# Optimization experiments

Measured on AMD Instinct MI355X. Metric: run time of the kernel, lower is better.

The kernel has to match this reference:

```python
import jax, jax.numpy as jnp
import numpy as np

N_NODES = 8192
D = 384
N_EDGES = 262144
N_REL = 4
N_LAYERS = 2
BATCH = 64


def setup_inputs() -> dict:
    key = jax.random.key(0)
    ks = jax.random.split(key, 8)
    x = jax.random.normal(ks[0], (N_NODES, D), jnp.float32)
    edge_index = jax.random.randint(ks[1], (2, N_EDGES), 0, N_NODES, dtype=jnp.int32)
    edge_type = jax.random.randint(ks[2], (N_EDGES,), 0, N_REL, dtype=jnp.int32)
    s = 1.0 / np.sqrt(D)
    W_rel = jax.random.uniform(ks[3], (N_LAYERS, N_REL, D, D), jnp.float32, -s, s)
    b_rel = jnp.zeros((N_LAYERS, N_REL, D), jnp.float32)
    norm_const = jnp.ones((N_LAYERS, N_REL), jnp.float32)
    W_msg = jax.random.uniform(ks[4], (N_LAYERS, D, D), jnp.float32, -s, s)
    b_msg = jnp.zeros((N_LAYERS, D), jnp.float32)
    W_self = jax.random.uniform(ks[5], (N_LAYERS, D, D), jnp.float32, -s, s)
    b_self = jnp.zeros((N_LAYERS, D), jnp.float32)
    bn_gamma = jnp.ones((D,), jnp.float32)
    bn_beta = jnp.zeros((D,), jnp.float32)
    return {"x": x, "edge_index": edge_index, "edge_type": edge_type,
            "bn_gamma": bn_gamma, "bn_beta": bn_beta,
            "W_rel": W_rel, "b_rel": b_rel, "norm_const": norm_const,
            "W_msg": W_msg, "b_msg": b_msg, "W_self": W_self, "b_self": b_self,
            "batch_size": BATCH}


def _seg_sum(v, idx, n):
    return jax.ops.segment_sum(v, idx, num_segments=n)


def _forward(x, bn_gamma, bn_beta, W_rel, b_rel, norm_const, W_msg, b_msg,
             W_self, b_self, edge_index, edge_type, batch_size):
    n = x.shape[0]
    # BatchNorm1d (training-mode batch stats) on the utterance embeddings
    mu = x.mean(axis=0)
    var = x.var(axis=0)
    h = bn_gamma * (x - mu) * jax.lax.rsqrt(var + 1e-5) + bn_beta
    src, dst = edge_index[0], edge_index[1]  # PyG: row=source(j), col=target(i)
    # pairwise cosine similarity, gathered only at the edges actually used:
    # edge_weights[dst, src] = <h_dst, h_src> / (|h_dst||h_src|)
    xn = h / jnp.linalg.norm(h, axis=1, keepdims=True)
    w_e = jnp.sum(xn[dst] * xn[src], axis=-1)  # [E]
    ones_e = jnp.ones(src.shape[0], jnp.float32)
    n_layers, n_rel = W_rel.shape[0], W_rel.shape[1]
    for l in range(n_layers):
        # RelationAwareMP: per-relation linear + weighted scatter-mean, summed
        out = jnp.zeros((n, W_rel.shape[2]), h.dtype)
        for r in range(n_rel):
            mask = (edge_type == r).astype(h.dtype)  # [E]
            xr = h @ W_rel[l, r].T + b_rel[l, r]  # [N, D]
            coef = mask * w_e / norm_const[l, r]  # [E]
            s = _seg_sum(coef[:, None] * xr[src], dst, n)
            c = _seg_sum(mask, dst, n)
            out = out + s / jnp.maximum(c, 1.0)[:, None]
        rel_out = jax.nn.relu(out)
        # MP: relu(mean_j lin(x_j) + self_lin(x)), then residual
        mj = rel_out @ W_msg[l].T + b_msg[l]
        s = _seg_sum(mj[src], dst, n)
        c = _seg_sum(ones_e, dst, n)
        aggr = s / jnp.maximum(c, 1.0)[:, None]
        h = jax.nn.relu(aggr + rel_out @ W_self[l].T + b_self[l]) + h
    return h.reshape(batch_size, -1, h.shape[-1]).mean(axis=1)


def reference(x, edge_index, edge_type, bn_gamma, bn_beta, W_rel, b_rel,
              norm_const, W_msg, b_msg, W_self, b_self, batch_size):
    return _forward(x, bn_gamma, bn_beta, W_rel, b_rel, norm_const,
                    W_msg, b_msg, W_self, b_self,
                    edge_index, edge_type, batch_size)
```

## Files before the change

### kernel.cpp

```cpp
#include <hip/hip_runtime.h>
#include <hip/hip_bf16.h>

#define NN 8192
#define DD 384
#define NE 262144
#define NR 4
#define NL 2
#define NB 64

typedef __attribute__((ext_vector_type(8))) short bf16x8;
typedef __attribute__((ext_vector_type(4))) float f32x4;

__device__ __forceinline__ unsigned short f2bf(float f) {
  unsigned u = __float_as_uint(f);
  unsigned r = (u + 0x7fffu + ((u >> 16) & 1u)) >> 16;
  return (unsigned short)r;
}
__device__ __forceinline__ unsigned pack_bf2(float lo, float hi) {
  return (unsigned)f2bf(lo) | ((unsigned)f2bf(hi) << 16);
}
__device__ __forceinline__ float bflo(unsigned u) { return __uint_as_float(u << 16); }
__device__ __forceinline__ float bfhi(unsigned u) { return __uint_as_float(u & 0xffff0000u); }
__device__ __forceinline__ void gl_lds16(const void* g, void* l) {
  __builtin_amdgcn_global_load_lds(
      (const __attribute__((address_space(1))) unsigned int*)g,
      (__attribute__((address_space(3))) unsigned int*)l, 16, 0, 0);
}
__device__ __forceinline__ float dot8(uint4 a, uint4 b) {
  return bflo(a.x) * bflo(b.x) + bfhi(a.x) * bfhi(b.x) +
         bflo(a.y) * bflo(b.y) + bfhi(a.y) * bfhi(b.y) +
         bflo(a.z) * bflo(b.z) + bfhi(a.z) * bfhi(b.z) +
         bflo(a.w) * bflo(b.w) + bfhi(a.w) * bfhi(b.w);
}

__global__ void k_colstats(const float* __restrict__ x, float* __restrict__ musum,
                           float* __restrict__ msqsum) {
  int c = threadIdx.x;
  int r0 = blockIdx.x * 32;
  float s = 0.f, s2 = 0.f;
  for (int r = 0; r < 32; ++r) {
    float v = x[(size_t)(r0 + r) * DD + c];
    s += v; s2 += v * v;
  }
  atomicAdd(&musum[c], s);
  atomicAdd(&msqsum[c], s2);
}

__global__ void k_bn(const float* __restrict__ x, const float* __restrict__ gamma,
                     const float* __restrict__ beta, const float* __restrict__ musum,
                     const float* __restrict__ msqsum, float* __restrict__ h,
                     short* __restrict__ h_bf, float* __restrict__ ninv) {
  int n = blockIdx.x;
  int t = threadIdx.x;
  float ss = 0.f;
#pragma unroll
  for (int i = 0; i < 6; ++i) {
    int c = t + i * 64;
    float m = musum[c] * (1.f / NN);
    float var = msqsum[c] * (1.f / NN) - m * m;
    float v = gamma[c] * (x[(size_t)n * DD + c] - m) * rsqrtf(var + 1e-5f) + beta[c];
    h[(size_t)n * DD + c] = v;
    h_bf[(size_t)n * DD + c] = (short)f2bf(v);
    ss += v * v;
  }
#pragma unroll
  for (int m = 32; m; m >>= 1) ss += __shfl_xor(ss, m, 64);
  if (t == 0) ninv[n] = rsqrtf(ss);
}

__global__ void k_counts(const int* __restrict__ ei, const int* __restrict__ et,
                         int* __restrict__ c_rel) {
  int e = blockIdx.x * blockDim.x + threadIdx.x;
  if (e >= NE) return;
  int dst = ei[NE + e];
  atomicAdd(&c_rel[dst * NR + et[e]], 1);
}

__global__ void k_scan(const int* __restrict__ c_rel, int* __restrict__ rp2,
                       int* __restrict__ cursor) {
  __shared__ int part[1024];
  int t = threadIdx.x;
  int base = t * 32;
  int v[32]; int s = 0;
#pragma unroll
  for (int i = 0; i < 32; ++i) { v[i] = c_rel[base + i]; s += v[i]; }
  part[t] = s;
  __syncthreads();
  for (int off = 1; off < 1024; off <<= 1) {
    int add = (t >= off) ? part[t - off] : 0;
    __syncthreads();
    part[t] += add;
    __syncthreads();
  }
  int run = (t == 0) ? 0 : part[t - 1];
  if (t == 0) rp2[0] = 0;
#pragma unroll
  for (int i = 0; i < 32; ++i) {
    cursor[base + i] = run;
    run += v[i];
    rp2[base + i + 1] = run;
  }
}

__global__ void k_we(const short* __restrict__ hb, const float* __restrict__ ninv,
                     const int* __restrict__ ei, float* __restrict__ w_e) {
  int sl = threadIdx.x & 15;
  int grp = (blockIdx.x * blockDim.x + threadIdx.x) >> 4;
  int ngrp = (gridDim.x * blockDim.x) >> 4;
  for (int e = grp; e < NE; e += ngrp) {
    int s = ei[e], d = ei[NE + e];
    const uint4* hs = (const uint4*)(hb + (size_t)s * DD);
    const uint4* hd = (const uint4*)(hb + (size_t)d * DD);
    uint4 a0 = hs[sl], a1 = hs[16 + sl], a2 = hs[32 + sl];
    uint4 b0 = hd[sl], b1 = hd[16 + sl], b2 = hd[32 + sl];
    float acc = dot8(a0, b0) + dot8(a1, b1) + dot8(a2, b2);
#pragma unroll
    for (int m = 8; m; m >>= 1) acc += __shfl_xor(acc, m, 64);
    if (sl == 0) w_e[e] = acc * ninv[s] * ninv[d];
  }
}

__global__ void k_fill(const int* __restrict__ ei, const int* __restrict__ et,
                       const float* __restrict__ w_e, int* __restrict__ cursor,
                       int* __restrict__ meta, float* __restrict__ wsort) {
  int e = blockIdx.x * blockDim.x + threadIdx.x;
  if (e >= NE) return;
  int src = ei[e], dst = ei[NE + e];
  int pos = atomicAdd(&cursor[dst * NR + et[e]], 1);
  meta[pos] = src;
  wsort[pos] = w_e[e];
}

__global__ void k_aggrel(const short* __restrict__ hb, const int* __restrict__ rp2,
                         const int* __restrict__ meta, const float* __restrict__ wsort,
                         const float* __restrict__ nc, short* __restrict__ Agg,
                         float* __restrict__ SC, int layer) {
  int n = blockIdx.x;
  int t = threadIdx.x;
  int r = t / 96;
  int i = t - r * 96;
  int beg = rp2[n * 4 + r], end = rp2[n * 4 + r + 1];
  float a0 = 0, a1 = 0, a2 = 0, a3 = 0, s = 0;
  int e = beg;
  for (; e + 3 < end; e += 4) {
    int s0 = meta[e], s1 = meta[e + 1], s2 = meta[e + 2], s3 = meta[e + 3];
    float w0 = wsort[e], w1 = wsort[e + 1], w2 = wsort[e + 2], w3 = wsort[e + 3];
    uint2 u0 = ((const uint2*)(hb + (size_t)s0 * DD))[i];
    uint2 u1 = ((const uint2*)(hb + (size_t)s1 * DD))[i];
    uint2 u2 = ((const uint2*)(hb + (size_t)s2 * DD))[i];
    uint2 u3 = ((const uint2*)(hb + (size_t)s3 * DD))[i];
    a0 += w0 * bflo(u0.x) + w1 * bflo(u1.x) + w2 * bflo(u2.x) + w3 * bflo(u3.x);
    a1 += w0 * bfhi(u0.x) + w1 * bfhi(u1.x) + w2 * bfhi(u2.x) + w3 * bfhi(u3.x);
    a2 += w0 * bflo(u0.y) + w1 * bflo(u1.y) + w2 * bflo(u2.y) + w3 * bflo(u3.y);
    a3 += w0 * bfhi(u0.y) + w1 * bfhi(u1.y) + w2 * bfhi(u2.y) + w3 * bfhi(u3.y);
    s += w0 + w1 + w2 + w3;
  }
  for (; e < end; ++e) {
    int s0 = meta[e];
    float w0 = wsort[e];
    uint2 u0 = ((const uint2*)(hb + (size_t)s0 * DD))[i];
    a0 += w0 * bflo(u0.x); a1 += w0 * bfhi(u0.x);
    a2 += w0 * bflo(u0.y); a3 += w0 * bfhi(u0.y);
    s += w0;
  }
  int c = end - beg;
  float f = 1.f / (nc[layer * 4 + r] * (float)(c > 1 ? c : 1));
  uint2 o;
  o.x = pack_bf2(a0 * f, a1 * f);
  o.y = pack_bf2(a2 * f, a3 * f);
  ((uint2*)(Agg + (size_t)n * 1536 + r * 384))[i] = o;
  if (i == 0) SC[n * 4 + r] = s * f;
}

__global__ void k_aggmp(short* __restrict__ B1, const int* __restrict__ rp2,
                        const int* __restrict__ meta) {
  __shared__ float red[3][96][4];
  int n = blockIdx.x;
  int t = threadIdx.x;
  int g = t / 96, i = t - g * 96;
  int beg = rp2[n * 4], end = rp2[n * 4 + 4];
  float a0 = 0, a1 = 0, a2 = 0, a3 = 0;
  int e = beg + g;
  for (; e + 12 < end; e += 16) {
    int s0 = meta[e], s1 = meta[e + 4], s2 = meta[e + 8], s3 = meta[e + 12];
    uint2 u0 = ((const uint2*)(B1 + (size_t)s0 * 768 + 384))[i];
    uint2 u1 = ((const uint2*)(B1 + (size_t)s1 * 768 + 384))[i];
    uint2 u2 = ((const uint2*)(B1 + (size_t)s2 * 768 + 384))[i];
    uint2 u3 = ((const uint2*)(B1 + (size_t)s3 * 768 + 384))[i];
    a0 += bflo(u0.x) + bflo(u1.x) + bflo(u2.x) + bflo(u3.x);
    a1 += bfhi(u0.x) + bfhi(u1.x) + bfhi(u2.x) + bfhi(u3.x);
    a2 += bflo(u0.y) + bflo(u1.y) + bflo(u2.y) + bflo(u3.y);
    a3 += bfhi(u0.y) + bfhi(u1.y) + bfhi(u2.y) + bfhi(u3.y);
  }
  for (; e < end; e += 4) {
    int s0 = meta[e];
    uint2 u = ((const uint2*)(B1 + (size_t)s0 * 768 + 384))[i];
    a0 += bflo(u.x); a1 += bfhi(u.x);
    a2 += bflo(u.y); a3 += bfhi(u.y);
  }
  if (g) {
    red[g - 1][i][0] = a0; red[g - 1][i][1] = a1;
    red[g - 1][i][2] = a2; red[g - 1][i][3] = a3;
  }
  __syncthreads();
  if (g == 0) {
#pragma unroll
    for (int k = 0; k < 3; ++k) {
      a0 += red[k][i][0]; a1 += red[k][i][1];
      a2 += red[k][i][2]; a3 += red[k][i][3];
    }
    float inv = (end > beg) ? 1.f / (float)(end - beg) : 0.f;
    uint2 o;
    o.x = pack_bf2(a0 * inv, a1 * inv);
    o.y = pack_bf2(a2 * inv, a3 * inv);
    ((uint2*)(B1 + (size_t)n * 768))[i] = o;
  }
}

__global__ void k_packall(const float* __restrict__ W_rel, const float* __restrict__ W_msg,
                          const float* __restrict__ W_self, short* __restrict__ Wcat,
                          short* __restrict__ Wcat2) {
  const int T1 = NL * 384 * 1536;
  const int T2 = NL * 384 * 768;
  int idx = blockIdx.x * blockDim.x + threadIdx.x;
  if (idx < T1) {
    int l = idx / (384 * 1536);
    int rem = idx - l * 384 * 1536;
    int i = rem / 1536, kk = rem - i * 1536;
    int r = kk / 384, k = kk - r * 384;
    Wcat[idx] = (short)f2bf(W_rel[(((size_t)(l * NR + r) * DD) + i) * DD + k]);
  } else if (idx < T1 + T2) {
    int j = idx - T1;
    int l = j / (384 * 768);
    int rem = j - l * 384 * 768;
    int i = rem / 768, kk = rem - i * 768;
    float v = (kk < 384) ? W_msg[((size_t)l * DD + i) * DD + kk]
                         : W_self[((size_t)l * DD + i) * DD + kk - 384];
    Wcat2[j] = (short)f2bf(v);
  }
}

template <int MODE>
__global__ __launch_bounds__(256) void k_gemm_mfma(
    const short* __restrict__ A, int K, const short* __restrict__ Bp,
    const float* __restrict__ SC, const float* __restrict__ brel_l,
    const float* __restrict__ bmsg_l, const float* __restrict__ bself_l,
    const int* __restrict__ rp2, float* __restrict__ h,
    short* __restrict__ h_bf, short* __restrict__ Cout) {
  __shared__ short As[64 * 32];
  __shared__ short Bs[64 * 32];
  int tid = threadIdx.x;
  int lane = tid & 63;
  int w = tid >> 6;
  int wr = w >> 1, wc = w & 1;
  int bm = blockIdx.x, bn = blockIdx.y;

  const short* Ag = A + (size_t)(bm * 64 + (tid >> 2)) * K + (tid & 3) * 8;
  const short* Bg = Bp + (size_t)(bn * 64 + (tid >> 2)) * K + (tid & 3) * 8;
  short* Asl = As + w * 512;
  short* Bsl = Bs + w * 512;

  f32x4 acc[2][2] = {};
  int fr = lane & 15, fk = (lane >> 4) * 8;
  for (int k0 = 0; k0 < K; k0 += 32) {
    __syncthreads();
    gl_lds16(Ag + k0, Asl);
    gl_lds16(Bg + k0, Bsl);
    __syncthreads();
    bf16x8 a[2], b[2];
#pragma unroll
    for (int i = 0; i < 2; ++i)
      a[i] = *(const bf16x8*)&As[(wr * 32 + i * 16 + fr) * 32 + fk];
#pragma unroll
    for (int j = 0; j < 2; ++j)
      b[j] = *(const bf16x8*)&Bs[(wc * 32 + j * 16 + fr) * 32 + fk];
#pragma unroll
    for (int i = 0; i < 2; ++i)
#pragma unroll
      for (int j = 0; j < 2; ++j)
        acc[i][j] = __builtin_amdgcn_mfma_f32_16x16x32_bf16(a[i], b[j], acc[i][j], 0, 0, 0);
  }

  int cr = (lane >> 4) * 4;
  int cc = lane & 15;
#pragma unroll
  for (int i = 0; i < 2; ++i) {
#pragma unroll
    for (int jj = 0; jj < 4; ++jj) {
      int row = bm * 64 + wr * 32 + i * 16 + cr + jj;
      if (MODE == 0) {
        float4 sc = *(const float4*)&SC[row * 4];
#pragma unroll
        for (int j = 0; j < 2; ++j) {
          int col = bn * 64 + wc * 32 + j * 16 + cc;
          float v = acc[i][j][jj] + sc.x * brel_l[col] + sc.y * brel_l[384 + col] +
                    sc.z * brel_l[768 + col] + sc.w * brel_l[1152 + col];
          Cout[(size_t)row * 768 + 384 + col] = (short)f2bf(fmaxf(v, 0.f));
        }
      } else {
        float bmul = (rp2[(row + 1) * 4] > rp2[row * 4]) ? 1.f : 0.f;
#pragma unroll
        for (int j = 0; j < 2; ++j) {
          int col = bn * 64 + wc * 32 + j * 16 + cc;
          float v = acc[i][j][jj] + bmul * bmsg_l[col] + bself_l[col];
          float o = fmaxf(v, 0.f) + h[(size_t)row * DD + col];
          h[(size_t)row * DD + col] = o;
          h_bf[(size_t)row * DD + col] = (short)f2bf(o);
        }
      }
    }
  }
}

__global__ void k_out(const float* __restrict__ h, float* __restrict__ out) {
  int b = blockIdx.x;
  int c = threadIdx.x;
  float s = 0.f;
  for (int j = 0; j < 128; ++j) s += h[(size_t)(b * 128 + j) * DD + c];
  out[b * DD + c] = s * (1.f / 128.f);
}

extern "C" void kernel_launch(void* const* d_in, const int* in_sizes, int n_in,
                              void* d_out, int out_size, void* d_ws, size_t ws_size,
                              hipStream_t stream) {
  const float* x      = (const float*)d_in[0];
  const int*   ei     = (const int*)d_in[1];
  const int*   et     = (const int*)d_in[2];
  const float* gamma  = (const float*)d_in[3];
  const float* beta   = (const float*)d_in[4];
  const float* W_rel  = (const float*)d_in[5];
  const float* b_rel  = (const float*)d_in[6];
  const float* nc     = (const float*)d_in[7];
  const float* W_msg  = (const float*)d_in[8];
  const float* b_msg  = (const float*)d_in[9];
  const float* W_self = (const float*)d_in[10];
  const float* b_self = (const float*)d_in[11];
  float* out = (float*)d_out;

  char* ws = (char*)d_ws;
  size_t off = 0;
  auto alloc = [&](size_t bytes) -> void* {
    void* p = ws + off;
    off = (off + bytes + 255) & ~(size_t)255;
    return p;
  };
  float* h      = (float*)alloc((size_t)NN * DD * 4);
  short* h_bf   = (short*)alloc((size_t)NN * DD * 2);
  short* Agg    = (short*)alloc((size_t)NN * 1536 * 2);
  short* B1     = (short*)alloc((size_t)NN * 768 * 2);
  short* Wcat   = (short*)alloc((size_t)NL * 384 * 1536 * 2);
  short* Wcat2  = (short*)alloc((size_t)NL * 384 * 768 * 2);
  float* SC     = (float*)alloc((size_t)NN * 4 * 4);
  float* w_e    = (float*)alloc((size_t)NE * 4);
  int*   meta   = (int*)alloc((size_t)NE * 4);
  float* wsort  = (float*)alloc((size_t)NE * 4);
  int*   rp2    = (int*)alloc((size_t)(NN * 4 + 1) * 4);
  int*   cursor = (int*)alloc((size_t)NN * 4 * 4);
  float* ninv   = (float*)alloc((size_t)NN * 4);
  char*  zb     = (char*)alloc(134144);
  float* musum  = (float*)(zb);
  float* msqsum = (float*)(zb + 1536);
  int*   c_rel  = (int*)(zb + 3072);

  hipMemsetAsync(zb, 0, 134144, stream);
  k_colstats<<<256, 384, 0, stream>>>(x, musum, msqsum);
  k_bn<<<NN, 64, 0, stream>>>(x, gamma, beta, musum, msqsum, h, h_bf, ninv);
  k_counts<<<NE / 256, 256, 0, stream>>>(ei, et, c_rel);
  k_scan<<<1, 1024, 0, stream>>>(c_rel, rp2, cursor);
  k_we<<<2048, 256, 0, stream>>>(h_bf, ninv, ei, w_e);
  k_fill<<<NE / 256, 256, 0, stream>>>(ei, et, w_e, cursor, meta, wsort);
  k_packall<<<(NL * 384 * 1536 + NL * 384 * 768 + 255) / 256, 256, 0, stream>>>(
      W_rel, W_msg, W_self, Wcat, Wcat2);

  for (int l = 0; l < NL; ++l) {
    k_aggrel<<<NN, 384, 0, stream>>>(h_bf, rp2, meta, wsort, nc, Agg, SC, l);
    k_gemm_mfma<0><<<dim3(128, 6), 256, 0, stream>>>(
        Agg, 1536, Wcat + (size_t)l * 384 * 1536, SC, b_rel + l * NR * DD,
        nullptr, nullptr, nullptr, nullptr, nullptr, B1);
    k_aggmp<<<NN, 384, 0, stream>>>(B1, rp2, meta);
    k_gemm_mfma<1><<<dim3(128, 6), 256, 0, stream>>>(
        B1, 768, Wcat2 + (size_t)l * 384 * 768, nullptr, nullptr,
        b_msg + l * DD, b_self + l * DD, rp2, h, h_bf, nullptr);
  }
  k_out<<<64, 384, 0, stream>>>(h, out);
}
```

Before: 328.7 us.

## Fuse edge-weight and CSR fill, widen GEMM K-tile with swizzled LDS, replace memset

Merges the edge cosine-weight kernel with the CSR fill kernel, so the weight is written straight into its sorted slot and the intermediate w_e buffer and one launch go away. The MFMA GEMM now stages 64-wide K tiles per iteration with an XOR-swizzled LDS layout, which halves the number of barrier pairs and is meant to avoid LDS bank conflicts. hipMemsetAsync is replaced by a small zeroing kernel to avoid memset API overhead. The fused kernel issues its atomics from a single lane per 16-lane group, which may serialise the fill, and the larger LDS tiles raise shared-memory use per block.

```diff
diff --git a/kernel.cpp b/kernel.cpp
--- a/kernel.cpp
+++ b/kernel.cpp
@@ -31,6 +31,11 @@
          bflo(a.y) * bflo(b.y) + bfhi(a.y) * bfhi(b.y) +
          bflo(a.z) * bflo(b.z) + bfhi(a.z) * bfhi(b.z) +
          bflo(a.w) * bflo(b.w) + bfhi(a.w) * bfhi(b.w);
+}
+
+__global__ void k_zero(uint4* __restrict__ p, int n4) {
+  int i = blockIdx.x * 256 + threadIdx.x;
+  if (i < n4) p[i] = make_uint4(0, 0, 0, 0);
 }
 
 __global__ void k_colstats(const float* __restrict__ x, float* __restrict__ musum,
@@ -102,8 +107,10 @@
   }
 }
 
-__global__ void k_we(const short* __restrict__ hb, const float* __restrict__ ninv,
-                     const int* __restrict__ ei, float* __restrict__ w_e) {
+__global__ void k_wefill(const short* __restrict__ hb, const float* __restrict__ ninv,
+                         const int* __restrict__ ei, const int* __restrict__ et,
+                         int* __restrict__ cursor, int* __restrict__ meta,
+                         float* __restrict__ wsort) {
   int sl = threadIdx.x & 15;
   int grp = (blockIdx.x * blockDim.x + threadIdx.x) >> 4;
   int ngrp = (gridDim.x * blockDim.x) >> 4;
@@ -116,19 +123,12 @@
     float acc = dot8(a0, b0) + dot8(a1, b1) + dot8(a2, b2);
 #pragma unroll
     for (int m = 8; m; m >>= 1) acc += __shfl_xor(acc, m, 64);
-    if (sl == 0) w_e[e] = acc * ninv[s] * ninv[d];
-  }
-}
-
-__global__ void k_fill(const int* __restrict__ ei, const int* __restrict__ et,
-                       const float* __restrict__ w_e, int* __restrict__ cursor,
-                       int* __restrict__ meta, float* __restrict__ wsort) {
-  int e = blockIdx.x * blockDim.x + threadIdx.x;
-  if (e >= NE) return;
-  int src = ei[e], dst = ei[NE + e];
-  int pos = atomicAdd(&cursor[dst * NR + et[e]], 1);
-  meta[pos] = src;
-  wsort[pos] = w_e[e];
+    if (sl == 0) {
+      int pos = atomicAdd(&cursor[d * NR + et[e]], 1);
+      meta[pos] = s;
+      wsort[pos] = acc * ninv[s] * ninv[d];
+    }
+  }
 }
 
 __global__ void k_aggrel(const short* __restrict__ hb, const int* __restrict__ rp2,
@@ -247,38 +247,55 @@
     const float* __restrict__ bmsg_l, const float* __restrict__ bself_l,
     const int* __restrict__ rp2, float* __restrict__ h,
     short* __restrict__ h_bf, short* __restrict__ Cout) {
-  __shared__ short As[64 * 32];
-  __shared__ short Bs[64 * 32];
+  __shared__ short As[64 * 64];
+  __shared__ short Bs[64 * 64];
   int tid = threadIdx.x;
   int lane = tid & 63;
   int w = tid >> 6;
   int wr = w >> 1, wc = w & 1;
   int bm = blockIdx.x, bn = blockIdx.y;
 
-  const short* Ag = A + (size_t)(bm * 64 + (tid >> 2)) * K + (tid & 3) * 8;
-  const short* Bg = Bp + (size_t)(bn * 64 + (tid >> 2)) * K + (tid & 3) * 8;
-  short* Asl = As + w * 512;
-  short* Bsl = Bs + w * 512;
+  int r0 = (w << 3) + (lane >> 3);
+  int qg = (lane & 7) ^ (r0 & 7);
+  const short* Ag0 = A + (size_t)(bm * 64 + r0) * K + qg * 8;
+  const short* Ag1 = A + (size_t)(bm * 64 + r0 + 32) * K + qg * 8;
+  const short* Bg0 = Bp + (size_t)(bn * 64 + r0) * K + qg * 8;
+  const short* Bg1 = Bp + (size_t)(bn * 64 + r0 + 32) * K + qg * 8;
+  short* Asl0 = As + w * 512;
+  short* Asl1 = As + 2048 + w * 512;
+  short* Bsl0 = Bs + w * 512;
+  short* Bsl1 = Bs + 2048 + w * 512;
 
   f32x4 acc[2][2] = {};
-  int fr = lane & 15, fk = (lane >> 4) * 8;
-  for (int k0 = 0; k0 < K; k0 += 32) {
+  int fr = lane & 15, fq = lane >> 4;
+  for (int k0 = 0; k0 < K; k0 += 64) {
     __syncthreads();
-    gl_lds16(Ag + k0, Asl);
-    gl_lds16(Bg + k0, Bsl);
+    gl_lds16(Ag0 + k0, Asl0);
+    gl_lds16(Ag1 + k0, Asl1);
+    gl_lds16(Bg0 + k0, Bsl0);
+    gl_lds16(Bg1 + k0, Bsl1);
     __syncthreads();
-    bf16x8 a[2], b[2];
-#pragma unroll
-    for (int i = 0; i < 2; ++i)
-      a[i] = *(const bf16x8*)&As[(wr * 32 + i * 16 + fr) * 32 + fk];
-#pragma unroll
-    for (int j = 0; j < 2; ++j)
-      b[j] = *(const bf16x8*)&Bs[(wc * 32 + j * 16 + fr) * 32 + fk];
-#pragma unroll
-    for (int i = 0; i < 2; ++i)
-#pragma unroll
-      for (int j = 0; j < 2; ++j)
-        acc[i][j] = __builtin_amdgcn_mfma_f32_16x16x32_bf16(a[i], b[j], acc[i][j], 0, 0, 0);
+#pragma unroll
+    for (int kk = 0; kk < 2; ++kk) {
+      bf16x8 a[2], b[2];
+#pragma unroll
+      for (int i = 0; i < 2; ++i) {
+        int r = wr * 32 + i * 16 + fr;
+        int qs = (kk * 4 + fq) ^ (r & 7);
+        a[i] = *(const bf16x8*)&As[r * 64 + qs * 8];
+      }
+#pragma unroll
+      for (int j = 0; j < 2; ++j) {
+        int r = wc * 32 + j * 16 + fr;
+        int qs = (kk * 4 + fq) ^ (r & 7);
+        b[j] = *(const bf16x8*)&Bs[r * 64 + qs * 8];
+      }
+#pragma unroll
+      for (int i = 0; i < 2; ++i)
+#pragma unroll
+        for (int j = 0; j < 2; ++j)
+          acc[i][j] = __builtin_amdgcn_mfma_f32_16x16x32_bf16(a[i], b[j], acc[i][j], 0, 0, 0);
+    }
   }
 
   int cr = (lane >> 4) * 4;
@@ -351,7 +368,6 @@
   short* Wcat   = (short*)alloc((size_t)NL * 384 * 1536 * 2);
   short* Wcat2  = (short*)alloc((size_t)NL * 384 * 768 * 2);
   float* SC     = (float*)alloc((size_t)NN * 4 * 4);
-  float* w_e    = (float*)alloc((size_t)NE * 4);
   int*   meta   = (int*)alloc((size_t)NE * 4);
   float* wsort  = (float*)alloc((size_t)NE * 4);
   int*   rp2    = (int*)alloc((size_t)(NN * 4 + 1) * 4);
@@ -362,13 +378,12 @@
   float* msqsum = (float*)(zb + 1536);
   int*   c_rel  = (int*)(zb + 3072);
 
-  hipMemsetAsync(zb, 0, 134144, stream);
+  k_zero<<<(134144 / 16 + 255) / 256, 256, 0, stream>>>((uint4*)zb, 134144 / 16);
   k_colstats<<<256, 384, 0, stream>>>(x, musum, msqsum);
   k_bn<<<NN, 64, 0, stream>>>(x, gamma, beta, musum, msqsum, h, h_bf, ninv);
   k_counts<<<NE / 256, 256, 0, stream>>>(ei, et, c_rel);
   k_scan<<<1, 1024, 0, stream>>>(c_rel, rp2, cursor);
-  k_we<<<2048, 256, 0, stream>>>(h_bf, ninv, ei, w_e);
-  k_fill<<<NE / 256, 256, 0, stream>>>(ei, et, w_e, cursor, meta, wsort);
+  k_wefill<<<2048, 256, 0, stream>>>(h_bf, ninv, ei, et, cursor, meta, wsort);
   k_packall<<<(NL * 384 * 1536 + NL * 384 * 768 + 255) / 256, 256, 0, stream>>>(
       W_rel, W_msg, W_self, Wcat, Wcat2);
 
```

Result: faster. 308.3 us (-6.2%).
